# Optimization experiments

Measured on AMD Instinct MI355X. Metric: run time of the kernel, lower is better.

Reference implementation:

```python
import jax, jax.numpy as jnp
import numpy as np

N = 10000   # num_nodes
U = 64      # num_units (rnn hidden per node)
DIN = 2     # input_dim per node
B = 16      # batch
E = 160000  # nnz of sparse support (avg degree 16)
D = DIN + U # concat feature size per node


def setup_inputs() -> dict:
    key = jax.random.key(0)
    ks = jax.random.split(key, 8)
    inputs = jax.random.normal(ks[0], (B, N * DIN), jnp.float32)
    hx = jax.random.normal(ks[1], (B, N * U), jnp.float32)
    # sparse support (scaled laplacian) in COO edge-list form
    rows = jax.random.randint(ks[2], (E,), 0, N, jnp.int32)
    cols = jax.random.randint(ks[3], (E,), 0, N, jnp.int32)
    vals = jax.random.normal(ks[4], (E,), jnp.float32) / 16.0
    # fc params: (input_size, 2*U), bias_start=1.0
    W_fc = jax.random.normal(ks[5], (D, 2 * U), jnp.float32) * (2.0 / (D + 2 * U)) ** 0.5
    b_fc = jnp.full((2 * U,), 1.0, jnp.float32)
    # gconv params: (input_size * num_matrices, U) with num_matrices = 2, bias_start=0.0
    W_g = jax.random.normal(ks[6], (2 * D, U), jnp.float32) * (2.0 / (2 * D + U)) ** 0.5
    b_g = jnp.zeros((U,), jnp.float32)
    return {"inputs": inputs, "hx": hx, "rows": rows, "cols": cols, "vals": vals,
            "W_fc": W_fc, "b_fc": b_fc, "W_g": W_g, "b_g": b_g}


def reference(inputs, hx, rows, cols, vals, W_fc, b_fc, W_g, b_g):
    # ---- gates via _fc (use_gc_for_ru=False), bias_start=1.0 ----
    xi = inputs.reshape(B * N, DIN)
    h = hx.reshape(B * N, U)
    cat = jnp.concatenate([xi, h], axis=-1)                  # (B*N, D)
    value = jax.nn.sigmoid(cat @ W_fc + b_fc)                # (B*N, 2U)
    value = value.reshape(B, N, 2 * U)
    r = value[..., :U].reshape(B, N * U)
    u = value[..., U:].reshape(B, N * U)

    # ---- candidate via _gconv(inputs, r*hx, U) ----
    xs = jnp.concatenate([inputs.reshape(B, N, DIN),
                          (r * hx).reshape(B, N, U)], axis=-1)  # (B, N, D)
    x0 = xs.transpose(1, 2, 0).reshape(N, D * B)             # (N, D*B)
    # sparse support matmul: x1 = S @ x0 via gather + segment_sum
    x1 = jax.ops.segment_sum(vals[:, None] * x0[cols], rows, num_segments=N)
    x = jnp.stack([x0, x1], axis=0)                          # (2, N, D*B)
    x = x.reshape(2, N, D, B).transpose(3, 1, 2, 0).reshape(B * N, D * 2)
    c = jnp.tanh(x @ W_g + b_g).reshape(B, N * U)            # activation = tanh

    # ---- GRU combine ----
    return u * hx + (1.0 - u) * c
```

## Files before the change

kernel.cpp:

```cpp
#include <hip/hip_runtime.h>

#define NN   10000
#define UU   64
#define DINP 2
#define BB   16
#define EE   160000
#define DCAT 66
#define LPAD 104
#define NPB  4
#define ECAP 64

typedef short short8 __attribute__((ext_vector_type(8)));
typedef float f32x4 __attribute__((ext_vector_type(4)));
typedef float f32x2 __attribute__((ext_vector_type(2)));

static __device__ __forceinline__ unsigned short f2bf(float f) {
  union { float f; unsigned u; } c; c.f = f;
  unsigned r = c.u + 0x7fffu + ((c.u >> 16) & 1u);
  return (unsigned short)(r >> 16);
}
static __device__ __forceinline__ float bfu2f(unsigned short h) {
  union { unsigned u; float f; } c; c.u = ((unsigned)h) << 16; return c.f;
}
static __device__ __forceinline__ float bf_lo(unsigned u) {
  union { unsigned u; float f; } c; c.u = u << 16; return c.f;
}
static __device__ __forceinline__ float bf_hi(unsigned u) {
  union { unsigned u; float f; } c; c.u = u & 0xffff0000u; return c.f;
}
static __device__ __forceinline__ float sigf(float x)   { return 1.0f / (1.0f + __expf(-x)); }
static __device__ __forceinline__ float tanh_f(float x) { return 2.0f / (1.0f + __expf(-2.0f * x)) - 1.0f; }

__global__ void k_scatter(const int* __restrict__ rows, const int* __restrict__ cols,
                          const float* __restrict__ vals, int* __restrict__ cnt,
                          int2* __restrict__ edges) {
  int e = blockIdx.x * 256 + threadIdx.x;
  if (e >= EE) return;
  int r = rows[e];
  int p = atomicAdd(&cnt[r], 1);
  if (p < ECAP) {
    union { float f; int i; } v; v.f = vals[e];
    edges[r * ECAP + p] = make_int2(cols[e], v.i);
  }
}

__global__ __launch_bounds__(256) void k1_gates_cand(
    const float* __restrict__ inp, const float* __restrict__ hx,
    const float* __restrict__ Wfc, const float* __restrict__ bfc_g,
    const float* __restrict__ Wg, const float* __restrict__ bg,
    unsigned* __restrict__ pack, unsigned* __restrict__ z8) {
  __shared__ unsigned short catb[16 * LPAD];
  __shared__ unsigned short xsl[16 * LPAD];

  const int tid = threadIdx.x;
  const int w = tid >> 6;
  const int lane = tid & 63;
  const int lr = lane & 15;
  const int lg = lane >> 4;
  const int jr = w * 16 + lr;

  for (int idx = tid; idx < 16 * (LPAD - DCAT); idx += 256) {
    int b = idx / (LPAD - DCAT), k = DCAT + idx % (LPAD - DCAT);
    catb[b * LPAD + k] = 0; xsl[b * LPAD + k] = 0;
  }
  const float bfc0 = bfc_g[jr];
  const float bfc1 = bfc_g[64 + jr];
  const float bgv  = bg[jr];

  short8 ffc0[3], ffc1[3], fg0r[3], fg1r[3];
#pragma unroll
  for (int c = 0; c < 3; ++c) {
#pragma unroll
    for (int e = 0; e < 8; ++e) {
      int k = c * 32 + lg * 8 + e;
      float v0 = 0.f, v1 = 0.f, g0 = 0.f, g1 = 0.f;
      if (k < DCAT) {
        v0 = Wfc[k * 128 + jr];
        v1 = Wfc[k * 128 + 64 + jr];
        g0 = Wg[(2 * k) * 64 + jr];
        g1 = Wg[(2 * k + 1) * 64 + jr];
      }
      ffc0[c][e] = (short)f2bf(v0); ffc1[c][e] = (short)f2bf(v1);
      fg0r[c][e] = (short)f2bf(g0); fg1r[c][e] = (short)f2bf(g1);
    }
  }

  const int n0 = blockIdx.x * NPB;
  float hv[4]; float xv = 0.f;
#pragma unroll
  for (int q = 0; q < 4; ++q) hv[q] = hx[(w * 4 + q) * (NN * UU) + n0 * UU + lane];
  if (w == 0 && lane < 32) xv = inp[(lane >> 1) * (NN * DINP) + n0 * DINP + (lane & 1)];
  __syncthreads();

  for (int i = 0; i < NPB; ++i) {
    const int n = n0 + i;
#pragma unroll
    for (int q = 0; q < 4; ++q)
      catb[(w * 4 + q) * LPAD + DINP + lane] = f2bf(hv[q]);
    unsigned short xv_bf = f2bf(xv);
    if (w == 0 && lane < 32)
      catb[(lane >> 1) * LPAD + (lane & 1)] = xv_bf;
    __syncthreads();

    short8 a0 = *(const short8*)&catb[lr * LPAD + 0  + lg * 8];
    short8 a1 = *(const short8*)&catb[lr * LPAD + 32 + lg * 8];
    short8 a2 = *(const short8*)&catb[lr * LPAD + 64 + lg * 8];
    f32x4 accr = {0.f, 0.f, 0.f, 0.f}, accu = {0.f, 0.f, 0.f, 0.f};
    accr = __builtin_amdgcn_mfma_f32_16x16x32_bf16(a0, ffc0[0], accr, 0, 0, 0);
    accu = __builtin_amdgcn_mfma_f32_16x16x32_bf16(a0, ffc1[0], accu, 0, 0, 0);
    accr = __builtin_amdgcn_mfma_f32_16x16x32_bf16(a1, ffc0[1], accr, 0, 0, 0);
    accu = __builtin_amdgcn_mfma_f32_16x16x32_bf16(a1, ffc1[1], accu, 0, 0, 0);
    accr = __builtin_amdgcn_mfma_f32_16x16x32_bf16(a2, ffc0[2], accr, 0, 0, 0);
    accu = __builtin_amdgcn_mfma_f32_16x16x32_bf16(a2, ffc1[2], accu, 0, 0, 0);

    if (w == 0 && lane < 32)
      xsl[(lane >> 1) * LPAD + (lane & 1)] = xv_bf;
    unsigned ub[4];
#pragma unroll
    for (int reg = 0; reg < 4; ++reg) {
      int b = lg * 4 + reg;
      float hvv = bfu2f(catb[b * LPAD + DINP + jr]);
      float r = sigf(accr[reg] + bfc0);
      xsl[b * LPAD + DINP + jr] = f2bf(r * hvv);
      ub[reg] = (unsigned)f2bf(sigf(accu[reg] + bfc1));
    }
    if (i + 1 < NPB) {
      int n2 = n + 1;
#pragma unroll
      for (int q = 0; q < 4; ++q) hv[q] = hx[(w * 4 + q) * (NN * UU) + n2 * UU + lane];
      if (w == 0 && lane < 32) xv = inp[(lane >> 1) * (NN * DINP) + n2 * DINP + (lane & 1)];
    }
    __syncthreads();

    short8 x0 = *(const short8*)&xsl[lr * LPAD + 0  + lg * 8];
    short8 x1 = *(const short8*)&xsl[lr * LPAD + 32 + lg * 8];
    short8 x2 = *(const short8*)&xsl[lr * LPAD + 64 + lg * 8];
    f32x4 accy = {0.f, 0.f, 0.f, 0.f}, accz = {0.f, 0.f, 0.f, 0.f};
    accy = __builtin_amdgcn_mfma_f32_16x16x32_bf16(x0, fg0r[0], accy, 0, 0, 0);
    accz = __builtin_amdgcn_mfma_f32_16x16x32_bf16(x0, fg1r[0], accz, 0, 0, 0);
    accy = __builtin_amdgcn_mfma_f32_16x16x32_bf16(x1, fg0r[1], accy, 0, 0, 0);
    accz = __builtin_amdgcn_mfma_f32_16x16x32_bf16(x1, fg1r[1], accz, 0, 0, 0);
    accy = __builtin_amdgcn_mfma_f32_16x16x32_bf16(x2, fg0r[2], accy, 0, 0, 0);
    accz = __builtin_amdgcn_mfma_f32_16x16x32_bf16(x2, fg1r[2], accz, 0, 0, 0);

#pragma unroll
    for (int reg = 0; reg < 4; ++reg) {
      int b = lg * 4 + reg;
      pack[b * (NN * UU) + n * UU + jr] =
          (((unsigned)f2bf(accy[reg] + bgv)) << 16) | ub[reg];
    }
    unsigned zw = (unsigned)__builtin_amdgcn_cvt_pk_fp8_f32(accz[0], accz[1], 0, 0);
    zw = (unsigned)__builtin_amdgcn_cvt_pk_fp8_f32(accz[2], accz[3], (int)zw, 1);
    z8[n * 256 + w * 64 + lg * 16 + lr] = zw;
  }
}

static __device__ __forceinline__ void load_edge(int i, int deg, const int2* ep,
                                                 const unsigned* zl,
                                                 uint4& z, float& v) {
  int ii = (i < deg) ? i : (deg - 1);
  int2 e = ep[ii];
  int col = __builtin_amdgcn_readfirstlane(e.x);
  int vb  = __builtin_amdgcn_readfirstlane(e.y);
  union { int i; float f; } cv; cv.i = vb;
  v = (i < deg) ? cv.f : 0.f;
  z = *(const uint4*)(zl + (size_t)col * 256);
}

static __device__ __forceinline__ void consume_edge(uint4 z, float v,
                                                    float (&acc)[4][4]) {
  unsigned zw[4] = {z.x, z.y, z.z, z.w};
#pragma unroll
  for (int q = 0; q < 4; ++q) {
    f32x2 lo = __builtin_amdgcn_cvt_pk_f32_fp8((int)zw[q], 0);
    f32x2 hi = __builtin_amdgcn_cvt_pk_f32_fp8((int)zw[q], 1);
    acc[q][0] += v * lo[0]; acc[q][1] += v * lo[1];
    acc[q][2] += v * hi[0]; acc[q][3] += v * hi[1];
  }
}

static __device__ __forceinline__ uint4 combine4(uint4 pk, float4 hv,
                                                 float a0, float a1,
                                                 float a2, float a3) {
  float aa[4] = {a0, a1, a2, a3};
  unsigned pkk[4] = {pk.x, pk.y, pk.z, pk.w};
  float hh[4] = {hv.x, hv.y, hv.z, hv.w};
  unsigned ov[4];
#pragma unroll
  for (int q = 0; q < 4; ++q) {
    float u = bf_lo(pkk[q]);
    float c = tanh_f(bf_hi(pkk[q]) + aa[q]);
    union { float f; unsigned u; } o;
    o.f = u * hh[q] + (1.f - u) * c;
    ov[q] = o.u;
  }
  return (uint4){ov[0], ov[1], ov[2], ov[3]};
}

__global__ __launch_bounds__(256) void k2_agg_combine(
    const int* __restrict__ cnt, const int2* __restrict__ edges,
    const unsigned* __restrict__ z8, const float* __restrict__ hx,
    unsigned* __restrict__ pack) {
  const int lane = threadIdx.x & 63;
  const int n = blockIdx.x * 4 + (threadIdx.x >> 6);
  const int jw = lane >> 4;
  const int lg = (lane >> 2) & 3;
  const int ja = lane & 3;
  const int jb = jw * 16 + ja * 4;

  const size_t f0 = (size_t)(lg * 4 + 0) * (NN * UU) + (size_t)n * UU + jb;
  const size_t f1 = f0 + (size_t)(NN * UU);
  const size_t f2 = f1 + (size_t)(NN * UU);
  const size_t f3 = f2 + (size_t)(NN * UU);
  uint4 pk0 = *(const uint4*)&pack[f0]; float4 hv0 = *(const float4*)&hx[f0];
  uint4 pk1 = *(const uint4*)&pack[f1]; float4 hv1 = *(const float4*)&hx[f1];
  uint4 pk2 = *(const uint4*)&pack[f2]; float4 hv2 = *(const float4*)&hx[f2];
  uint4 pk3 = *(const uint4*)&pack[f3]; float4 hv3 = *(const float4*)&hx[f3];

  float acc[4][4];
#pragma unroll
  for (int q = 0; q < 4; ++q)
#pragma unroll
    for (int m = 0; m < 4; ++m) acc[q][m] = 0.f;

  const int deg = cnt[n];
  const int2* ep = edges + n * ECAP;
  const unsigned* zl = z8 + (size_t)lane * 4;

  if (deg > 0) {
    uint4 zA, zB; float vA, vB;
    load_edge(0, deg, ep, zl, zA, vA);
    load_edge(1, deg, ep, zl, zB, vB);
    for (int s = 0; s < deg; s += 2) {
      uint4 zC, zD; float vC, vD;
      load_edge(s + 2, deg, ep, zl, zC, vC);
      load_edge(s + 3, deg, ep, zl, zD, vD);
      consume_edge(zA, vA, acc);
      consume_edge(zB, vB, acc);
      zA = zC; vA = vC; zB = zD; vB = vD;
    }
  }

  *(uint4*)&pack[f0] = combine4(pk0, hv0, acc[0][0], acc[1][0], acc[2][0], acc[3][0]);
  *(uint4*)&pack[f1] = combine4(pk1, hv1, acc[0][1], acc[1][1], acc[2][1], acc[3][1]);
  *(uint4*)&pack[f2] = combine4(pk2, hv2, acc[0][2], acc[1][2], acc[2][2], acc[3][2]);
  *(uint4*)&pack[f3] = combine4(pk3, hv3, acc[0][3], acc[1][3], acc[2][3], acc[3][3]);
}

extern "C" void kernel_launch(void* const* d_in, const int* in_sizes, int n_in,
                              void* d_out, int out_size, void* d_ws, size_t ws_size,
                              hipStream_t stream) {
  const float* inp  = (const float*)d_in[0];
  const float* hx   = (const float*)d_in[1];
  const int*   rows = (const int*)d_in[2];
  const int*   cols = (const int*)d_in[3];
  const float* vals = (const float*)d_in[4];
  const float* Wfc  = (const float*)d_in[5];
  const float* bfc  = (const float*)d_in[6];
  const float* Wg   = (const float*)d_in[7];
  const float* bg   = (const float*)d_in[8];
  unsigned* pack = (unsigned*)d_out;

  char* ws = (char*)d_ws;
  unsigned* z8  = (unsigned*)(ws + 0);
  int*  cnt     = (int*)(ws + 10240000);
  int2* edges   = (int2*)(ws + 10280064);

  hipMemsetAsync(cnt, 0, NN * sizeof(int), stream);
  k_scatter<<<(EE + 255) / 256, 256, 0, stream>>>(rows, cols, vals, cnt, edges);
  k1_gates_cand<<<NN / NPB, 256, 0, stream>>>(inp, hx, Wfc, bfc, Wg, bg, pack, z8);
  k2_agg_combine<<<NN / 4, 256, 0, stream>>>(cnt, edges, z8, hx, pack);
}
```

Before: 181.9 us.

## Load MFMA A-operands directly from global and deepen edge-gather prefetch

The gate GEMM's A operands now come straight from global hx/inputs into registers in MFMA layout, with the weight rows permuted so hidden units come first and the input features last. This removes the catb shared staging buffer and one barrier per node. The r*h tile is double-buffered in a smaller shared array, and the input-feature fragment is reused for the candidate GEMM. The sparse gather loop now prefetches four edges ahead instead of two, and the degree is clamped to ECAP, which trades extra registers for more memory-level parallelism.

New measurement: 195.9 us. +7.7%, slower.

```diff
diff --git a/kernel.cpp b/kernel.cpp
--- a/kernel.cpp
+++ b/kernel.cpp
@@ -6,7 +6,7 @@
 #define BB   16
 #define EE   160000
 #define DCAT 66
-#define LPAD 104
+#define XST  72
 #define NPB  4
 #define ECAP 64
 
@@ -18,9 +18,6 @@
   union { float f; unsigned u; } c; c.f = f;
   unsigned r = c.u + 0x7fffu + ((c.u >> 16) & 1u);
   return (unsigned short)(r >> 16);
-}
-static __device__ __forceinline__ float bfu2f(unsigned short h) {
-  union { unsigned u; float f; } c; c.u = ((unsigned)h) << 16; return c.f;
 }
 static __device__ __forceinline__ float bf_lo(unsigned u) {
   union { unsigned u; float f; } c; c.u = u << 16; return c.f;
@@ -49,8 +46,7 @@
     const float* __restrict__ Wfc, const float* __restrict__ bfc_g,
     const float* __restrict__ Wg, const float* __restrict__ bg,
     unsigned* __restrict__ pack, unsigned* __restrict__ z8) {
-  __shared__ unsigned short catb[16 * LPAD];
-  __shared__ unsigned short xsl[16 * LPAD];
+  __shared__ unsigned short xsl[2][16 * XST];
 
   const int tid = threadIdx.x;
   const int w = tid >> 6;
@@ -59,10 +55,6 @@
   const int lg = lane >> 4;
   const int jr = w * 16 + lr;
 
-  for (int idx = tid; idx < 16 * (LPAD - DCAT); idx += 256) {
-    int b = idx / (LPAD - DCAT), k = DCAT + idx % (LPAD - DCAT);
-    catb[b * LPAD + k] = 0; xsl[b * LPAD + k] = 0;
-  }
   const float bfc0 = bfc_g[jr];
   const float bfc1 = bfc_g[64 + jr];
   const float bgv  = bg[jr];
@@ -74,11 +66,17 @@
     for (int e = 0; e < 8; ++e) {
       int k = c * 32 + lg * 8 + e;
       float v0 = 0.f, v1 = 0.f, g0 = 0.f, g1 = 0.f;
-      if (k < DCAT) {
-        v0 = Wfc[k * 128 + jr];
-        v1 = Wfc[k * 128 + 64 + jr];
-        g0 = Wg[(2 * k) * 64 + jr];
-        g1 = Wg[(2 * k + 1) * 64 + jr];
+      if (k < 64) {
+        v0 = Wfc[(k + 2) * 128 + jr];
+        v1 = Wfc[(k + 2) * 128 + 64 + jr];
+        g0 = Wg[(2 * k + 4) * 64 + jr];
+        g1 = Wg[(2 * k + 5) * 64 + jr];
+      } else if (k < 66) {
+        int kk = k - 64;
+        v0 = Wfc[kk * 128 + jr];
+        v1 = Wfc[kk * 128 + 64 + jr];
+        g0 = Wg[(2 * kk) * 64 + jr];
+        g1 = Wg[(2 * kk + 1) * 64 + jr];
       }
       ffc0[c][e] = (short)f2bf(v0); ffc1[c][e] = (short)f2bf(v1);
       fg0r[c][e] = (short)f2bf(g0); fg1r[c][e] = (short)f2bf(g1);
@@ -86,25 +84,36 @@
   }
 
   const int n0 = blockIdx.x * NPB;
-  float hv[4]; float xv = 0.f;
-#pragma unroll
-  for (int q = 0; q < 4; ++q) hv[q] = hx[(w * 4 + q) * (NN * UU) + n0 * UU + lane];
-  if (w == 0 && lane < 32) xv = inp[(lane >> 1) * (NN * DINP) + n0 * DINP + (lane & 1)];
-  __syncthreads();
+  const float* hrow = hx + (size_t)lr * (NN * UU);
+  const float* irow = inp + (size_t)lr * (NN * DINP);
+
+  float4 h0, h1, h2, h3; float2 xf = {0.f, 0.f}; float hj[4];
+  {
+    const float* hp = hrow + (size_t)n0 * UU;
+    h0 = *(const float4*)&hp[lg * 8];      h1 = *(const float4*)&hp[lg * 8 + 4];
+    h2 = *(const float4*)&hp[32 + lg * 8]; h3 = *(const float4*)&hp[32 + lg * 8 + 4];
+    if (lg == 0) xf = *(const float2*)&irow[(size_t)n0 * DINP];
+#pragma unroll
+    for (int reg = 0; reg < 4; ++reg)
+      hj[reg] = hx[(size_t)(lg * 4 + reg) * (NN * UU) + (size_t)n0 * UU + jr];
+  }
 
   for (int i = 0; i < NPB; ++i) {
     const int n = n0 + i;
-#pragma unroll
-    for (int q = 0; q < 4; ++q)
-      catb[(w * 4 + q) * LPAD + DINP + lane] = f2bf(hv[q]);
-    unsigned short xv_bf = f2bf(xv);
-    if (w == 0 && lane < 32)
-      catb[(lane >> 1) * LPAD + (lane & 1)] = xv_bf;
-    __syncthreads();
-
-    short8 a0 = *(const short8*)&catb[lr * LPAD + 0  + lg * 8];
-    short8 a1 = *(const short8*)&catb[lr * LPAD + 32 + lg * 8];
-    short8 a2 = *(const short8*)&catb[lr * LPAD + 64 + lg * 8];
+    unsigned short* xb = &xsl[i & 1][0];
+
+    short8 a0, a1, a2;
+    a0[0] = (short)f2bf(h0.x); a0[1] = (short)f2bf(h0.y);
+    a0[2] = (short)f2bf(h0.z); a0[3] = (short)f2bf(h0.w);
+    a0[4] = (short)f2bf(h1.x); a0[5] = (short)f2bf(h1.y);
+    a0[6] = (short)f2bf(h1.z); a0[7] = (short)f2bf(h1.w);
+    a1[0] = (short)f2bf(h2.x); a1[1] = (short)f2bf(h2.y);
+    a1[2] = (short)f2bf(h2.z); a1[3] = (short)f2bf(h2.w);
+    a1[4] = (short)f2bf(h3.x); a1[5] = (short)f2bf(h3.y);
+    a1[6] = (short)f2bf(h3.z); a1[7] = (short)f2bf(h3.w);
+    a2 = (short8){0, 0, 0, 0, 0, 0, 0, 0};
+    a2[0] = (short)f2bf(xf.x); a2[1] = (short)f2bf(xf.y);
+
     f32x4 accr = {0.f, 0.f, 0.f, 0.f}, accu = {0.f, 0.f, 0.f, 0.f};
     accr = __builtin_amdgcn_mfma_f32_16x16x32_bf16(a0, ffc0[0], accr, 0, 0, 0);
     accu = __builtin_amdgcn_mfma_f32_16x16x32_bf16(a0, ffc1[0], accu, 0, 0, 0);
@@ -113,35 +122,40 @@
     accr = __builtin_amdgcn_mfma_f32_16x16x32_bf16(a2, ffc0[2], accr, 0, 0, 0);
     accu = __builtin_amdgcn_mfma_f32_16x16x32_bf16(a2, ffc1[2], accu, 0, 0, 0);
 
-    if (w == 0 && lane < 32)
-      xsl[(lane >> 1) * LPAD + (lane & 1)] = xv_bf;
+    float4 nh0 = h0, nh1 = h1, nh2 = h2, nh3 = h3;
+    float2 nxf = xf; float nhj[4];
+#pragma unroll
+    for (int reg = 0; reg < 4; ++reg) nhj[reg] = hj[reg];
+    if (i + 1 < NPB) {
+      const int n2 = n + 1;
+      const float* hp = hrow + (size_t)n2 * UU;
+      nh0 = *(const float4*)&hp[lg * 8];      nh1 = *(const float4*)&hp[lg * 8 + 4];
+      nh2 = *(const float4*)&hp[32 + lg * 8]; nh3 = *(const float4*)&hp[32 + lg * 8 + 4];
+      if (lg == 0) nxf = *(const float2*)&irow[(size_t)n2 * DINP];
+#pragma unroll
+      for (int reg = 0; reg < 4; ++reg)
+        nhj[reg] = hx[(size_t)(lg * 4 + reg) * (NN * UU) + (size_t)n2 * UU + jr];
+    }
+
     unsigned ub[4];
 #pragma unroll
     for (int reg = 0; reg < 4; ++reg) {
       int b = lg * 4 + reg;
-      float hvv = bfu2f(catb[b * LPAD + DINP + jr]);
       float r = sigf(accr[reg] + bfc0);
-      xsl[b * LPAD + DINP + jr] = f2bf(r * hvv);
+      xb[b * XST + jr] = f2bf(r * hj[reg]);
       ub[reg] = (unsigned)f2bf(sigf(accu[reg] + bfc1));
     }
-    if (i + 1 < NPB) {
-      int n2 = n + 1;
-#pragma unroll
-      for (int q = 0; q < 4; ++q) hv[q] = hx[(w * 4 + q) * (NN * UU) + n2 * UU + lane];
-      if (w == 0 && lane < 32) xv = inp[(lane >> 1) * (NN * DINP) + n2 * DINP + (lane & 1)];
-    }
     __syncthreads();
 
-    short8 x0 = *(const short8*)&xsl[lr * LPAD + 0  + lg * 8];
-    short8 x1 = *(const short8*)&xsl[lr * LPAD + 32 + lg * 8];
-    short8 x2 = *(const short8*)&xsl[lr * LPAD + 64 + lg * 8];
+    short8 x0v = *(const short8*)&xb[lr * XST + lg * 8];
+    short8 x1v = *(const short8*)&xb[lr * XST + 32 + lg * 8];
     f32x4 accy = {0.f, 0.f, 0.f, 0.f}, accz = {0.f, 0.f, 0.f, 0.f};
-    accy = __builtin_amdgcn_mfma_f32_16x16x32_bf16(x0, fg0r[0], accy, 0, 0, 0);
-    accz = __builtin_amdgcn_mfma_f32_16x16x32_bf16(x0, fg1r[0], accz, 0, 0, 0);
-    accy = __builtin_amdgcn_mfma_f32_16x16x32_bf16(x1, fg0r[1], accy, 0, 0, 0);
-    accz = __builtin_amdgcn_mfma_f32_16x16x32_bf16(x1, fg1r[1], accz, 0, 0, 0);
-    accy = __builtin_amdgcn_mfma_f32_16x16x32_bf16(x2, fg0r[2], accy, 0, 0, 0);
-    accz = __builtin_amdgcn_mfma_f32_16x16x32_bf16(x2, fg1r[2], accz, 0, 0, 0);
+    accy = __builtin_amdgcn_mfma_f32_16x16x32_bf16(x0v, fg0r[0], accy, 0, 0, 0);
+    accz = __builtin_amdgcn_mfma_f32_16x16x32_bf16(x0v, fg1r[0], accz, 0, 0, 0);
+    accy = __builtin_amdgcn_mfma_f32_16x16x32_bf16(x1v, fg0r[1], accy, 0, 0, 0);
+    accz = __builtin_amdgcn_mfma_f32_16x16x32_bf16(x1v, fg1r[1], accz, 0, 0, 0);
+    accy = __builtin_amdgcn_mfma_f32_16x16x32_bf16(a2,  fg0r[2], accy, 0, 0, 0);
+    accz = __builtin_amdgcn_mfma_f32_16x16x32_bf16(a2,  fg1r[2], accz, 0, 0, 0);
 
 #pragma unroll
     for (int reg = 0; reg < 4; ++reg) {
@@ -152,6 +166,10 @@
     unsigned zw = (unsigned)__builtin_amdgcn_cvt_pk_fp8_f32(accz[0], accz[1], 0, 0);
     zw = (unsigned)__builtin_amdgcn_cvt_pk_fp8_f32(accz[2], accz[3], (int)zw, 1);
     z8[n * 256 + w * 64 + lg * 16 + lr] = zw;
+
+    h0 = nh0; h1 = nh1; h2 = nh2; h3 = nh3; xf = nxf;
+#pragma unroll
+    for (int reg = 0; reg < 4; ++reg) hj[reg] = nhj[reg];
   }
 }
 
@@ -223,21 +241,29 @@
 #pragma unroll
     for (int m = 0; m < 4; ++m) acc[q][m] = 0.f;
 
-  const int deg = cnt[n];
+  int deg = cnt[n];
+  deg = (deg < ECAP) ? deg : ECAP;
   const int2* ep = edges + n * ECAP;
   const unsigned* zl = z8 + (size_t)lane * 4;
 
   if (deg > 0) {
-    uint4 zA, zB; float vA, vB;
+    uint4 zA, zB, zC, zD; float vA, vB, vC, vD;
     load_edge(0, deg, ep, zl, zA, vA);
     load_edge(1, deg, ep, zl, zB, vB);
-    for (int s = 0; s < deg; s += 2) {
-      uint4 zC, zD; float vC, vD;
-      load_edge(s + 2, deg, ep, zl, zC, vC);
-      load_edge(s + 3, deg, ep, zl, zD, vD);
+    load_edge(2, deg, ep, zl, zC, vC);
+    load_edge(3, deg, ep, zl, zD, vD);
+    for (int s = 0; s < deg; s += 4) {
+      uint4 zE, zF, zG, zH; float vE, vF, vG, vH;
+      load_edge(s + 4, deg, ep, zl, zE, vE);
+      load_edge(s + 5, deg, ep, zl, zF, vF);
+      load_edge(s + 6, deg, ep, zl, zG, vG);
+      load_edge(s + 7, deg, ep, zl, zH, vH);
       consume_edge(zA, vA, acc);
       consume_edge(zB, vB, acc);
-      zA = zC; vA = vC; zB = zD; vB = vD;
+      consume_edge(zC, vC, acc);
+      consume_edge(zD, vD, acc);
+      zA = zE; vA = vE; zB = zF; vB = vF;
+      zC = zG; vC = vG; zD = zH; vD = vH;
     }
   }
 
```
